# Kernel optimization log

Measured on AMD Instinct MI355X. Metric: run time of the kernel, lower is better.

Reference implementation:

```python
import jax, jax.numpy as jnp
import numpy as np

T_ENC = 80
MAX_LEN = 80
B = 64
D_IN = 4096
EU = 1024
DU = 1024
VOCAB = 20000
ATT = 80


def _lstm_scan(xs, h0, c0, W_ih, W_hh, b_ih, b_hh):
    """Single-layer LSTM over leading time dim. xs: [T,B,I]. Returns (ys[T,B,H], hT, cT)."""
    def step(carry, x):
        h, c = carry
        g = x @ W_ih.T + b_ih + h @ W_hh.T + b_hh
        i, f, gg, o = jnp.split(g, 4, axis=-1)
        c = jax.nn.sigmoid(f) * c + jax.nn.sigmoid(i) * jnp.tanh(gg)
        h = jax.nn.sigmoid(o) * jnp.tanh(c)
        return (h, c), h
    (hT, cT), ys = jax.lax.scan(step, (h0, c0), xs)
    return ys, hT, cT


def setup_inputs() -> dict:
    key = jax.random.key(0)
    ks = jax.random.split(key, 20)
    s = 0.05
    inp = {
        "input_data": jax.random.normal(ks[0], (T_ENC, B, D_IN), jnp.float32),
        "correct_answer": jax.random.normal(ks[1], (MAX_LEN, B, VOCAB), jnp.float32),
        # encoder LSTM params (torch gate order i,f,g,o)
        "enc_W_ih": jax.random.normal(ks[2], (4 * EU, D_IN), jnp.float32) * s,
        "enc_W_hh": jax.random.normal(ks[3], (4 * EU, EU), jnp.float32) * s,
        "enc_b_ih": jax.random.normal(ks[4], (4 * EU,), jnp.float32) * s,
        "enc_b_hh": jax.random.normal(ks[5], (4 * EU,), jnp.float32) * s,
        # decoder LSTM: input = decoder_unit + encoder_unit
        "dec_W_ih": jax.random.normal(ks[6], (4 * DU, DU + EU), jnp.float32) * s,
        "dec_W_hh": jax.random.normal(ks[7], (4 * DU, DU), jnp.float32) * s,
        "dec_b_ih": jax.random.normal(ks[8], (4 * DU,), jnp.float32) * s,
        "dec_b_hh": jax.random.normal(ks[9], (4 * DU,), jnp.float32) * s,
        # embeddings
        "in_emb_W": jax.random.normal(ks[10], (DU, VOCAB), jnp.float32) * s,
        "in_emb_b": jax.random.normal(ks[11], (DU,), jnp.float32) * s,
        "out_emb_W": jax.random.normal(ks[12], (VOCAB, DU), jnp.float32) * s,
        "out_emb_b": jax.random.normal(ks[13], (VOCAB,), jnp.float32) * s,
        # attention: linear_l1du_max ((d_l+1)*d_u -> 80), linear_2du_du (2*d_u -> d_u)
        "att_W1": jax.random.normal(ks[14], (ATT, 2 * DU), jnp.float32) * s,
        "att_b1": jax.random.normal(ks[15], (ATT,), jnp.float32) * s,
        "att_W2": jax.random.normal(ks[16], (DU, 2 * DU), jnp.float32) * s,
        "att_b2": jax.random.normal(ks[17], (DU,), jnp.float32) * s,
        "prelu_w": jnp.full((1,), 0.25, jnp.float32),  # PReLU(num_parameters=1) init
        "max_len": 80,
        "real_ans_length": jax.random.randint(ks[18], (B,), 0, 80),
    }
    return inp


def reference(input_data, correct_answer,
              enc_W_ih, enc_W_hh, enc_b_ih, enc_b_hh,
              dec_W_ih, dec_W_hh, dec_b_ih, dec_b_hh,
              in_emb_W, in_emb_b, out_emb_W, out_emb_b,
              att_W1, att_b1, att_W2, att_b2, prelu_w,
              max_len, real_ans_length):
    z_eh = jnp.zeros((B, EU), jnp.float32)
    z_dh = jnp.zeros((B, DU), jnp.float32)

    # encoding stage
    enc_seq, enc_h, enc_c = _lstm_scan(input_data, z_eh, z_eh, enc_W_ih, enc_W_hh, enc_b_ih, enc_b_hh)
    pad_tag = jnp.zeros((input_data.shape[0], B, DU), jnp.float32)
    dec_in0 = jnp.concatenate([enc_seq, pad_tag], axis=2)
    dec_out_seq, dec_h, dec_c = _lstm_scan(dec_in0, z_dh, z_dh, dec_W_ih, dec_W_hh, dec_b_ih, dec_b_hh)

    # encoder over zero padding inputs (continues encoder state)
    pad_in = jnp.zeros((max_len, B, D_IN), jnp.float32)
    enc_pad_seq, _, _ = _lstm_scan(pad_in, enc_h, enc_c, enc_W_ih, enc_W_hh, enc_b_ih, enc_b_hh)

    # teacher-forced samples (schedule_sample_rate == 1 -> always ground truth)
    bos = jnp.zeros((B, VOCAB), jnp.float32).at[:, -2].set(1.0)
    sample0 = bos @ in_emb_W.T + in_emb_b                              # [B, DU]
    samples_rest = correct_answer[1:max_len] @ in_emb_W.T + in_emb_b  # [max_len-1, B, DU]
    samples = jnp.concatenate([sample0[None], samples_rest], axis=0)   # [max_len, B, DU]

    E = enc_seq  # [80, B, EU]; attention weights have exactly 80 slots

    def dec_step(carry, inp):
        h, c = carry
        sample, enc_pad = inp
        # Attention: i = h (single layer), a = concat(i, word)
        a = jnp.concatenate([h, sample], axis=-1)          # [B, 2*DU]
        w = jax.nn.softmax(a @ att_W1.T + att_b1, axis=1)  # [B, 80]
        f = jnp.einsum('bs,sbh->bh', w, E)                 # [B, EU]
        cc = jnp.concatenate([sample, f], axis=-1)         # [B, 2*DU]
        z = cc @ att_W2.T + att_b2
        o = jnp.where(z >= 0, z, prelu_w[0] * z)           # PReLU (scalar param)
        context = o + enc_pad                              # [B, EU]
        x = jnp.concatenate([sample, context], axis=-1)    # [B, DU+EU]
        g = x @ dec_W_ih.T + dec_b_ih + h @ dec_W_hh.T + dec_b_hh
        gi, gf, gg, go = jnp.split(g, 4, axis=-1)
        c = jax.nn.sigmoid(gf) * c + jax.nn.sigmoid(gi) * jnp.tanh(gg)
        h = jax.nn.sigmoid(go) * jnp.tanh(c)
        word = h @ out_emb_W.T + out_emb_b                 # [B, VOCAB]
        return (h, c), word

    (_, _), words = jax.lax.scan(dec_step, (dec_h, dec_c), (samples, enc_pad_seq))
    return words  # [max_len, B, VOCAB]
```

## Files before the change

### kernel.cpp

```cpp
#include <hip/hip_runtime.h>
#include <cstddef>
#include <cstdint>

typedef __attribute__((ext_vector_type(8))) short short8v;
typedef __attribute__((ext_vector_type(4))) float f32x4;

__device__ __forceinline__ float sigmf(float x) { return 1.0f / (1.0f + __expf(-x)); }

__device__ __forceinline__ unsigned short bf16_rn(float x) {
    union { float f; unsigned u; } v; v.f = x;
    unsigned r = v.u + 0x7FFF + ((v.u >> 16) & 1);
    return (unsigned short)(r >> 16);
}
__device__ __forceinline__ float bf16_to_f(unsigned short h) {
    union { unsigned u; float f; } v; v.u = ((unsigned)h) << 16; return v.f;
}
__device__ __forceinline__ unsigned long long pack4(unsigned short a, unsigned short b,
                                                    unsigned short c, unsigned short d) {
    return (unsigned long long)a | ((unsigned long long)b << 16)
         | ((unsigned long long)c << 32) | ((unsigned long long)d << 48);
}

#define MFMA_(d, va, vb) d = __builtin_amdgcn_mfma_f32_16x16x32_bf16(va, vb, d, 0, 0, 0)

#define AT_LD(p)        __hip_atomic_load((p), __ATOMIC_RELAXED, __HIP_MEMORY_SCOPE_AGENT)
#define AT_ST(p, v)     __hip_atomic_store((p), (v), __ATOMIC_RELAXED, __HIP_MEMORY_SCOPE_AGENT)
#define AT_ST_REL(p, v) __hip_atomic_store((p), (v), __ATOMIC_RELEASE, __HIP_MEMORY_SCOPE_AGENT)
#define AT_ADD(p, v)    __hip_atomic_fetch_add((p), (v), __ATOMIC_RELAXED, __HIP_MEMORY_SCOPE_AGENT)

__device__ __forceinline__ void write_frag3_nt(unsigned short* __restrict__ dst, int NRGW,
                                               int r, int k, float x)
{
    unsigned short hi = bf16_rn(x); float r1 = x - bf16_to_f(hi);
    unsigned short md = bf16_rn(r1);
    unsigned short lo = bf16_rn(r1 - bf16_to_f(md));
    int base = (((r >> 4) * 32 + (k >> 5)) * 64 + ((k >> 3) & 3) * 16 + (r & 15)) * 8 + (k & 7);
    int ps = NRGW * 16384;
    __builtin_nontemporal_store(hi, &dst[base]);
    __builtin_nontemporal_store(md, &dst[ps + base]);
    __builtin_nontemporal_store(lo, &dst[2 * ps + base]);
}

__launch_bounds__(256)
__global__ void rearr_frag(const float* __restrict__ src, int ld, int c0,
                           unsigned short* __restrict__ dst, int R, int K)
{
    int idx = blockIdx.x * 256 + threadIdx.x;
    int kpr = K >> 3;
    if (idx >= R * kpr) return;
    int r = idx / kpr, k = (idx % kpr) * 8;
    int NRGW = R >> 4;
    const float* s = src + (size_t)r * ld + c0 + k;
    float4 v0 = *(const float4*)s, v1 = *(const float4*)(s + 4);
    float xs[8] = {v0.x, v0.y, v0.z, v0.w, v1.x, v1.y, v1.z, v1.w};
    unsigned short hi[8], md[8], lo[8];
#pragma unroll
    for (int e = 0; e < 8; ++e) {
        hi[e] = bf16_rn(xs[e]); float r1 = xs[e] - bf16_to_f(hi[e]);
        md[e] = bf16_rn(r1);
        lo[e] = bf16_rn(r1 - bf16_to_f(md[e]));
    }
    int base = (((r >> 4) * 32 + (k >> 5)) * 64 + ((k >> 3) & 3) * 16 + (r & 15)) * 8;
    size_t ps = (size_t)NRGW * 16384;
    *(unsigned long long*)&dst[base]          = pack4(hi[0], hi[1], hi[2], hi[3]);
    *(unsigned long long*)&dst[base + 4]      = pack4(hi[4], hi[5], hi[6], hi[7]);
    *(unsigned long long*)&dst[ps + base]     = pack4(md[0], md[1], md[2], md[3]);
    *(unsigned long long*)&dst[ps + base + 4] = pack4(md[4], md[5], md[6], md[7]);
    *(unsigned long long*)&dst[2*ps + base]     = pack4(lo[0], lo[1], lo[2], lo[3]);
    *(unsigned long long*)&dst[2*ps + base + 4] = pack4(lo[4], lo[5], lo[6], lo[7]);
}

__device__ __forceinline__ void tree_barrier(unsigned* bar, int gidx, int ng, int bpg)
{
    __syncthreads();
    if (threadIdx.x == 0) {
        unsigned* gcnt = bar + gidx * 32;
        unsigned* ggen = bar + gidx * 32 + 1;
        unsigned* rcnt = bar + ng * 32;
        unsigned* rgen = bar + ng * 32 + 1;
        __threadfence();
        unsigned mygen = AT_LD(ggen);
        unsigned prev = AT_ADD(gcnt, 1u);
        if (prev == (unsigned)(bpg - 1)) {
            AT_ST(gcnt, 0u);
            unsigned rg = AT_LD(rgen);
            unsigned rprev = AT_ADD(rcnt, 1u);
            if (rprev == (unsigned)(ng - 1)) {
                AT_ST(rcnt, 0u);
                AT_ST_REL(rgen, rg + 1u);
            } else {
                while (AT_LD(rgen) == rg) __builtin_amdgcn_s_sleep(1);
            }
            AT_ST_REL(ggen, mygen + 1u);
        } else {
            while (AT_LD(ggen) == mygen) __builtin_amdgcn_s_sleep(1);
        }
        __threadfence();
    }
    __syncthreads();
}

template <int NS>
__launch_bounds__(256, 2)
__global__ void gemm_mfma_split(const float* __restrict__ A, int lda,
                                const float* __restrict__ W, int ldw,
                                float* __restrict__ C, int ldc,
                                const float* __restrict__ bias,
                                int M, int N, int K)
{
    __shared__ unsigned short Abf[NS][128][40];
    __shared__ unsigned short Bbf[NS][128][40];
    const int tid = threadIdx.x;
    const int m0 = blockIdx.y * 128, n0 = blockIdx.x * 128;
    const int wave = tid >> 6, lane = tid & 63;
    const int wr = wave >> 1, wc = wave & 1;
    const int lr = lane & 15, lk = (lane >> 4) * 8;

    f32x4 acc[4][4];
#pragma unroll
    for (int i = 0; i < 4; ++i)
#pragma unroll
        for (int j = 0; j < 4; ++j) acc[i][j] = (f32x4){0.f, 0.f, 0.f, 0.f};

    const int arow = tid >> 1;
    const int akh  = (tid & 1) * 16;
    int gr = m0 + arow; if (gr > M - 1) gr = M - 1;
    int gn = n0 + arow; if (gn > N - 1) gn = N - 1;
    const float* aptr = A + (size_t)gr * lda + akh;
    const float* wptr = W + (size_t)gn * ldw + akh;

    for (int k0 = 0; k0 < K; k0 += 32) {
#pragma unroll
        for (int q = 0; q < 4; ++q) {
            float4 v = *(const float4*)(aptr + k0 + q * 4);
            float xs[4] = {v.x, v.y, v.z, v.w};
            unsigned short h[4], hm[4], hl[4];
#pragma unroll
            for (int e = 0; e < 4; ++e) {
                h[e] = bf16_rn(xs[e]);
                if (NS == 3) {
                    float r1 = xs[e] - bf16_to_f(h[e]);
                    hm[e] = bf16_rn(r1);
                    hl[e] = bf16_rn(r1 - bf16_to_f(hm[e]));
                }
            }
            *(unsigned long long*)&Abf[0][arow][akh + q * 4] = pack4(h[0], h[1], h[2], h[3]);
            if (NS == 3) {
                *(unsigned long long*)&Abf[1][arow][akh + q * 4] = pack4(hm[0], hm[1], hm[2], hm[3]);
                *(unsigned long long*)&Abf[2][arow][akh + q * 4] = pack4(hl[0], hl[1], hl[2], hl[3]);
            }
        }
#pragma unroll
        for (int q = 0; q < 4; ++q) {
            float4 v = *(const float4*)(wptr + k0 + q * 4);
            float xs[4] = {v.x, v.y, v.z, v.w};
            unsigned short h[4], hm[4], hl[4];
#pragma unroll
            for (int e = 0; e < 4; ++e) {
                h[e] = bf16_rn(xs[e]);
                if (NS == 3) {
                    float r1 = xs[e] - bf16_to_f(h[e]);
                    hm[e] = bf16_rn(r1);
                    hl[e] = bf16_rn(r1 - bf16_to_f(hm[e]));
                }
            }
            *(unsigned long long*)&Bbf[0][arow][akh + q * 4] = pack4(h[0], h[1], h[2], h[3]);
            if (NS == 3) {
                *(unsigned long long*)&Bbf[1][arow][akh + q * 4] = pack4(hm[0], hm[1], hm[2], hm[3]);
                *(unsigned long long*)&Bbf[2][arow][akh + q * 4] = pack4(hl[0], hl[1], hl[2], hl[3]);
            }
        }
        __syncthreads();

        short8v a[NS][4], b[4];
#pragma unroll
        for (int p = 0; p < NS; ++p)
#pragma unroll
            for (int i = 0; i < 4; ++i)
                a[p][i] = *(const short8v*)&Abf[p][wr * 64 + i * 16 + lr][lk];
#pragma unroll
        for (int q = 0; q < NS; ++q) {
#pragma unroll
            for (int j = 0; j < 4; ++j)
                b[j] = *(const short8v*)&Bbf[q][wc * 64 + j * 16 + lr][lk];
            const int pmax = (NS == 1) ? 1 : (3 - q);
#pragma unroll
            for (int p = 0; p < 3; ++p) {
                if (p >= pmax) break;
#pragma unroll
                for (int i = 0; i < 4; ++i)
#pragma unroll
                    for (int j = 0; j < 4; ++j)
                        acc[i][j] = __builtin_amdgcn_mfma_f32_16x16x32_bf16(
                            a[p][i], b[j], acc[i][j], 0, 0, 0);
            }
        }
        __syncthreads();
    }

    const int crow = (lane >> 4) * 4;
#pragma unroll
    for (int i = 0; i < 4; ++i) {
        int mbase = m0 + wr * 64 + i * 16 + crow;
#pragma unroll
        for (int j = 0; j < 4; ++j) {
            int n = n0 + wc * 64 + j * 16 + lr;
            if (n < N) {
                float bv = bias[n];
#pragma unroll
                for (int r = 0; r < 4; ++r) {
                    int m = mbase + r;
                    if (m < M) C[(size_t)m * ldc + n] = acc[i][j][r] + bv;
                }
            }
        }
    }
}

__launch_bounds__(256)
__global__ void zero_f(float* __restrict__ p, int n)
{
    int i = blockIdx.x * 256 + threadIdx.x;
    if (i < n) p[i] = 0.f;
}

__launch_bounds__(256)
__global__ void vec_add2(const float* __restrict__ a, const float* __restrict__ b,
                         float* __restrict__ o, int n)
{
    int i = blockIdx.x * 256 + threadIdx.x;
    if (i < n) o[i] = a[i] + b[i];
}

__launch_bounds__(256)
__global__ void sample0_fill(const float* __restrict__ emW, const float* __restrict__ emb,
                             float* __restrict__ samples)
{
    int idx = blockIdx.x * 256 + threadIdx.x;
    int d = idx & 1023;
    samples[idx] = emW[(size_t)d * 20000 + 19998] + emb[d];
}

__device__ __forceinline__ void stage_A(unsigned short* __restrict__ LDSA,
                                        const unsigned short* __restrict__ src,
                                        int rg, int tid)
{
#pragma unroll
    for (int p = 0; p < 3; ++p) {
        const unsigned short* sp = src + (size_t)(p * 4 + rg) * 16384;
        unsigned short* dp = LDSA + p * 16384;
#pragma unroll
        for (int it = 0; it < 4; ++it) {
            int idx = tid + it * 512;
            *(short8v*)&dp[idx * 8] = *(const short8v*)&sp[idx * 8];
        }
    }
}

__device__ __forceinline__ f32x4 mfma16(const unsigned short* __restrict__ LDSA,
                                        const short8v* __restrict__ wreg,
                                        int kh, int lane)
{
    f32x4 acc0 = (f32x4){0.f,0.f,0.f,0.f}, acc1 = acc0;
#pragma unroll
    for (int i = 0; i < 16; ++i) {
        int kf = kh * 16 + i;
        short8v a0 = *(const short8v*)&LDSA[(kf * 64 + lane) * 8];
        short8v a1 = *(const short8v*)&LDSA[16384 + (kf * 64 + lane) * 8];
        short8v a2 = *(const short8v*)&LDSA[32768 + (kf * 64 + lane) * 8];
        short8v b0 = wreg[i * 3 + 0], b1 = wreg[i * 3 + 1], b2 = wreg[i * 3 + 2];
        f32x4& A = (i & 1) ? acc1 : acc0;
        MFMA_(A, a0, b0); MFMA_(A, a0, b1); MFMA_(A, a1, b0);
        MFMA_(A, a1, b1); MFMA_(A, a0, b2); MFMA_(A, a2, b0);
    }
    return acc0 + acc1;
}

__launch_bounds__(512, 1)
__attribute__((amdgpu_waves_per_eu(1, 2)))
__global__ void coop_enc80(const unsigned short* __restrict__ WencF,
                           const float* __restrict__ Xbig,
                           unsigned short* __restrict__ hfrag,
                           float* __restrict__ enc_seq,
                           float* __restrict__ cglobE,
                           unsigned* __restrict__ bar)
{
    __shared__ unsigned short LDSA[3 * 16384];
    __shared__ float gbuf[8][16][16];
    const int bid = blockIdx.x, tid = threadIdx.x;
    const int w = tid >> 6, lane = tid & 63;
    const int g = w & 3, kh = w >> 2;
    const int rg = bid & 3, cg = bid >> 2;
    const int wbase = g * 64 + cg;
    const int r_l = (tid & 255) >> 4, c_l = tid & 15;
    const int row = rg * 16 + r_l, col = cg * 16 + c_l;
    float cstate = 0.f;

    short8v wreg[48];
#pragma unroll
    for (int i = 0; i < 16; ++i) {
        int kf = kh * 16 + i;
#pragma unroll
        for (int p = 0; p < 3; ++p)
            wreg[i * 3 + p] = *(const short8v*)&WencF[((size_t)(p * 256 + wbase) * 32 + kf) * 512 + lane * 8];
    }

    float pf[4];
    if (tid < 256) {
#pragma unroll
        for (int g2 = 0; g2 < 4; ++g2)
            pf[g2] = Xbig[(size_t)row * 4096 + g2 * 1024 + col];
    }

    for (int s = 0; s < 80; ++s) {
        const unsigned short* hf = hfrag + (s & 1) * 196608;
        stage_A(LDSA, hf, rg, tid);
        __syncthreads();
        f32x4 acc = mfma16(LDSA, wreg, kh, lane);
#pragma unroll
        for (int r = 0; r < 4; ++r)
            gbuf[w][(lane >> 4) * 4 + r][lane & 15] = acc[r];
        __syncthreads();

        if (tid < 256) {
            float gv[4];
#pragma unroll
            for (int g2 = 0; g2 < 4; ++g2)
                gv[g2] = gbuf[g2][r_l][c_l] + gbuf[4 + g2][r_l][c_l] + pf[g2];
            float cn = sigmf(gv[1]) * cstate + sigmf(gv[0]) * tanhf(gv[2]);
            float hn = sigmf(gv[3]) * tanhf(cn);
            cstate = cn;
            __builtin_nontemporal_store(hn, &enc_seq[(size_t)s * 65536 + row * 1024 + col]);
            write_frag3_nt(hfrag + ((s + 1) & 1) * 196608, 4, row, col, hn);
            if (s == 79) __builtin_nontemporal_store(cstate, &cglobE[row * 1024 + col]);
            else {
#pragma unroll
                for (int g2 = 0; g2 < 4; ++g2)
                    pf[g2] = Xbig[((size_t)(s + 1) * 64 + row) * 4096 + g2 * 1024 + col];
            }
        }
        tree_barrier(bar, bid >> 5, 8, 32);
    }
}

__launch_bounds__(512, 1)
__attribute__((amdgpu_waves_per_eu(1, 2)))
__global__ void coop_padwarm(const unsigned short* __restrict__ WencF,
                             const unsigned short* __restrict__ WdecF,
                             const float* __restrict__ benc,
                             const float* __restrict__ Xwarm,
                             const float* __restrict__ cglobE,
                             unsigned short* __restrict__ hfragE,
                             unsigned short* __restrict__ hfragD,
                             float* __restrict__ enc_pad,
                             float* __restrict__ cglobD,
                             float* __restrict__ h_fp32,
                             unsigned* __restrict__ barE,
                             unsigned* __restrict__ barW)
{
    __shared__ unsigned short LDSA[3 * 16384];
    __shared__ float gbuf[8][16][16];
    const int bid = blockIdx.x, tid = threadIdx.x;
    const int w = tid >> 6, lane = tid & 63;
    const int g = w & 3, kh = w >> 2;
    const bool isW = bid >= 128;
    const int lb = bid & 127;
    const int rg2 = lb & 1, cg = lb >> 1;
    const int wbase = g * 64 + cg;
    const int r_l = (tid & 255) >> 4, c_l = tid & 15;
    const int col = cg * 16 + c_l;
    const unsigned short* Wf = isW ? WdecF : WencF;
    unsigned short* hfrag = isW ? hfragD : hfragE;
    unsigned* bar = isW ? barW : barE;

    short8v wreg[48];
#pragma unroll
    for (int i = 0; i < 16; ++i) {
        int kf = kh * 16 + i;
#pragma unroll
        for (int p = 0; p < 3; ++p)
            wreg[i * 3 + p] = *(const short8v*)&Wf[((size_t)(p * 256 + wbase) * 32 + kf) * 512 + lane * 8];
    }

    float cst[2] = {0.f, 0.f};
    float pfx[2][4];
    if (tid < 256) {
#pragma unroll
        for (int l = 0; l < 2; ++l) {
            int row = rg2 * 32 + l * 16 + r_l;
            if (!isW) cst[l] = cglobE[row * 1024 + col];
#pragma unroll
            for (int g2 = 0; g2 < 4; ++g2)
                pfx[l][g2] = isW ? Xwarm[(size_t)row * 4096 + g2 * 1024 + col]
                                 : benc[g2 * 1024 + col];
        }
    }

    for (int s = 0; s < 80; ++s) {
        const unsigned short* hf = hfrag + (s & 1) * 196608;
        unsigned short* hout = hfrag + ((s + 1) & 1) * 196608;
#pragma unroll
        for (int l = 0; l < 2; ++l) {
            const int rgi = rg2 * 2 + l;
            stage_A(LDSA, hf, rgi, tid);
            __syncthreads();
            f32x4 acc = mfma16(LDSA, wreg, kh, lane);
#pragma unroll
            for (int r = 0; r < 4; ++r)
                gbuf[w][(lane >> 4) * 4 + r][lane & 15] = acc[r];
            __syncthreads();
            if (tid < 256) {
                const int row = rgi * 16 + r_l;
                float gv[4];
#pragma unroll
                for (int g2 = 0; g2 < 4; ++g2)
                    gv[g2] = gbuf[g2][r_l][c_l] + gbuf[4 + g2][r_l][c_l] + pfx[l][g2];
                float cn = sigmf(gv[1]) * cst[l] + sigmf(gv[0]) * tanhf(gv[2]);
                float hn = sigmf(gv[3]) * tanhf(cn);
                cst[l] = cn;
                if (!isW)
                    __builtin_nontemporal_store(hn, &enc_pad[(size_t)s * 65536 + row * 1024 + col]);
                write_frag3_nt(hout, 4, row, col, hn);
                if (isW) {
                    if (s == 79) {
                        __builtin_nontemporal_store(hn, &h_fp32[row * 1024 + col]);
                        __builtin_nontemporal_store(cn, &cglobD[row * 1024 + col]);
                    } else {
#pragma unroll
                        for (int g2 = 0; g2 < 4; ++g2)
                            pfx[l][g2] = Xwarm[((size_t)(s + 1) * 64 + row) * 4096 + g2 * 1024 + col];
                    }
                }
            }
            __syncthreads();
        }
        tree_barrier(bar, (lb >> 5), 4, 32);
    }
}

__launch_bounds__(512, 2)
__global__ void coop_dec80(const unsigned short* __restrict__ WihcF,
                           const unsigned short* __restrict__ WhhF,
                           const float* __restrict__ W1,
                           const float* __restrict__ EW2,
                           const float* __restrict__ S_g,
                           const float* __restrict__ ctxS,
                           const float* __restrict__ S_log,
                           const float* __restrict__ enc_pad,
                           const float* __restrict__ prelu_w,
                           const float* __restrict__ h_fp32,
                           const float* __restrict__ cglobD,
                           unsigned short* __restrict__ hfrag,
                           unsigned short* __restrict__ ctxfrag,
                           float* __restrict__ h_all,
                           float* __restrict__ gsum,
                           unsigned* __restrict__ bar)
{
    __shared__ float EW2T[80 * 256];
    __shared__ float gred[8][1024];
    __shared__ float hfull[1024];
    __shared__ float wsm[80];
    __shared__ float rbuf[128];
    const int bid = blockIdx.x, tid = threadIdx.x;
    const int w = tid >> 6, lane = tid & 63;
    const int gg = bid >> 6, cg = bid & 63;
    const int wbase = gg * 64 + cg;
    const int kq = w;
    const int b = bid >> 2, jc = bid & 3;
    const float pw = prelu_w[0];

    const unsigned short* Wsrc = (kq < 4) ? WihcF : WhhF;
    const int kfbase = (kq & 3) * 8;
    short8v wreg[24];
#pragma unroll
    for (int i = 0; i < 8; ++i) {
#pragma unroll
        for (int p = 0; p < 3; ++p)
            wreg[i * 3 + p] = *(const short8v*)&Wsrc[((size_t)(p * 256 + wbase) * 32 + kfbase + i) * 512 + lane * 8];
    }

    float c2[2];
    c2[0] = cglobD[b * 1024 + tid * 2];
    c2[1] = cglobD[b * 1024 + tid * 2 + 1];

    for (int i = tid; i < 80 * 256; i += 512) {
        int ss = i >> 8, j = i & 255;
        EW2T[i] = EW2[((size_t)ss * 64 + b) * 1024 + jc * 256 + j];
    }

    for (int i = tid; i < 1024; i += 512) hfull[i] = h_fp32[b * 1024 + i];
    __syncthreads();
    {
#pragma unroll
        for (int i = 0; i < 10; ++i) {
            int sx = w * 10 + i;
            float p = 0.f;
#pragma unroll
            for (int q = 0; q < 16; ++q)
                p = fmaf(hfull[lane + q * 64], W1[(size_t)sx * 2048 + lane + q * 64], p);
#pragma unroll
            for (int off = 32; off; off >>= 1) p += __shfl_down(p, off, 64);
            if (lane == 0) wsm[sx] = p + S_log[(size_t)b * 80 + sx];
        }
        __syncthreads();
        float v = (tid < 80) ? wsm[tid] : -3.4e38f;
        if (tid < 128) rbuf[tid] = v;
        __syncthreads();
        for (int off = 64; off >= 1; off >>= 1) {
            if (tid < off) rbuf[tid] = fmaxf(rbuf[tid], rbuf[tid + off]);
            __syncthreads();
        }
        float mx = rbuf[0];
        __syncthreads();
        float e = (tid < 80) ? __expf(wsm[tid] - mx) : 0.f;
        if (tid < 128) rbuf[tid] = e;
        __syncthreads();
        for (int off = 64; off >= 1; off >>= 1) {
            if (tid < off) rbuf[tid] += rbuf[tid + off];
            __syncthreads();
        }
        float inv = 1.f / rbuf[0];
        __syncthreads();
        if (tid < 80) wsm[tid] = e * inv;
        __syncthreads();
        if (tid < 256) {
            float f = 0.f;
#pragma unroll 8
            for (int ss = 0; ss < 80; ++ss)
                f = fmaf(wsm[ss], EW2T[ss * 256 + tid], f);
            int col = jc * 256 + tid;
            float val = f + ctxS[(size_t)b * 1024 + col];
            val = (val >= 0.f) ? val : pw * val;
            val += enc_pad[(size_t)b * 1024 + col];
            write_frag3_nt(ctxfrag, 4, b, col, val);
        }
    }
    tree_barrier(bar, bid >> 5, 8, 32);

    for (int t = 0; t < 80; ++t) {
        const int s = 80 + t;
        unsigned short* hout = hfrag + ((s + 1) & 1) * 196608;
        const unsigned short* hf = hfrag + (s & 1) * 196608;

        float pf2[2][4];
        {
            const float* xb = S_g + ((size_t)t * 64 + b) * 4096;
#pragma unroll
            for (int e = 0; e < 2; ++e) {
                int col = tid * 2 + e;
#pragma unroll
                for (int g2 = 0; g2 < 4; ++g2) pf2[e][g2] = xb[g2 * 1024 + col];
            }
        }

        {
            f32x4 acc[4];
#pragma unroll
            for (int rg = 0; rg < 4; ++rg) acc[rg] = (f32x4){0.f,0.f,0.f,0.f};
            const unsigned short* asrc = (kq < 4) ? ctxfrag : hf;
#pragma unroll
            for (int i = 0; i < 8; ++i) {
                int kfl = kfbase + i;
#pragma unroll
                for (int rg = 0; rg < 4; ++rg) {
                    const unsigned short* ab = asrc + ((size_t)rg * 32 + kfl) * 512 + lane * 8;
                    short8v a0 = *(const short8v*)&ab[0];
                    short8v a1 = *(const short8v*)&ab[65536];
                    short8v a2 = *(const short8v*)&ab[131072];
                    short8v b0 = wreg[i * 3 + 0], b1 = wreg[i * 3 + 1], b2 = wreg[i * 3 + 2];
                    MFMA_(acc[rg], a0, b0); MFMA_(acc[rg], a0, b1); MFMA_(acc[rg], a1, b0);
                    MFMA_(acc[rg], a1, b1); MFMA_(acc[rg], a0, b2); MFMA_(acc[rg], a2, b0);
                }
            }
#pragma unroll
            for (int rg = 0; rg < 4; ++rg)
#pragma unroll
                for (int r = 0; r < 4; ++r)
                    gred[w][rg * 256 + lane * 4 + r] = acc[rg][r];
            __syncthreads();
#pragma unroll
            for (int e2 = 0; e2 < 2; ++e2) {
                int slot = tid * 2 + e2;
                int rg = slot >> 8, l = (slot >> 2) & 63, r = slot & 3;
                float sum = 0.f;
#pragma unroll
                for (int w2 = 0; w2 < 8; ++w2) sum += gred[w2][slot];
                int row = rg * 16 + (l >> 4) * 4 + r;
                int col = cg * 16 + (l & 15);
                __builtin_nontemporal_store(sum, &gsum[((size_t)gg * 64 + row) * 1024 + col]);
            }
        }
        tree_barrier(bar, bid >> 5, 8, 32);

        {
            float hv[2];
#pragma unroll
            for (int e = 0; e < 2; ++e) {
                int col = tid * 2 + e;
                float gv[4];
#pragma unroll
                for (int g2 = 0; g2 < 4; ++g2)
                    gv[g2] = gsum[((size_t)g2 * 64 + b) * 1024 + col] + pf2[e][g2];
                float cn = sigmf(gv[1]) * c2[e] + sigmf(gv[0]) * tanhf(gv[2]);
                float hn = sigmf(gv[3]) * tanhf(cn);
                c2[e] = cn;
                hfull[col] = hn;
                hv[e] = hn;
            }
            __syncthreads();
            if (tid >= jc * 128 && tid < (jc + 1) * 128) {
#pragma unroll
                for (int e = 0; e < 2; ++e) {
                    int col = tid * 2 + e;
                    __builtin_nontemporal_store(hv[e], &h_all[((size_t)t * 64 + b) * 1024 + col]);
                    write_frag3_nt(hout, 4, b, col, hv[e]);
                }
            }
            if (t < 79) {
#pragma unroll
                for (int i = 0; i < 10; ++i) {
                    int sx = w * 10 + i;
                    float p = 0.f;
#pragma unroll
                    for (int q = 0; q < 16; ++q)
                        p = fmaf(hfull[lane + q * 64], W1[(size_t)sx * 2048 + lane + q * 64], p);
#pragma unroll
                    for (int off = 32; off; off >>= 1) p += __shfl_down(p, off, 64);
                    if (lane == 0) wsm[sx] = p + S_log[((size_t)(t + 1) * 64 + b) * 80 + sx];
                }
                __syncthreads();
                float v = (tid < 80) ? wsm[tid] : -3.4e38f;
                if (tid < 128) rbuf[tid] = v;
                __syncthreads();
                for (int off = 64; off >= 1; off >>= 1) {
                    if (tid < off) rbuf[tid] = fmaxf(rbuf[tid], rbuf[tid + off]);
                    __syncthreads();
                }
                float mx = rbuf[0];
                __syncthreads();
                float e = (tid < 80) ? __expf(wsm[tid] - mx) : 0.f;
                if (tid < 128) rbuf[tid] = e;
                __syncthreads();
                for (int off = 64; off >= 1; off >>= 1) {
                    if (tid < off) rbuf[tid] += rbuf[tid + off];
                    __syncthreads();
                }
                float inv = 1.f / rbuf[0];
                __syncthreads();
                if (tid < 80) wsm[tid] = e * inv;
                __syncthreads();
                if (tid < 256) {
                    float f = 0.f;
#pragma unroll 8
                    for (int ss = 0; ss < 80; ++ss)
                        f = fmaf(wsm[ss], EW2T[ss * 256 + tid], f);
                    int col = jc * 256 + tid;
                    float val = f + ctxS[((size_t)(t + 1) * 64 + b) * 1024 + col];
                    val = (val >= 0.f) ? val : pw * val;
                    val += enc_pad[((size_t)(t + 1) * 64 + b) * 1024 + col];
                    write_frag3_nt(ctxfrag, 4, b, col, val);
                }
            }
        }
        tree_barrier(bar, bid >> 5, 8, 32);
    }
}

extern "C" void kernel_launch(void* const* d_in, const int* in_sizes, int n_in,
                              void* d_out, int out_size, void* d_ws, size_t ws_size,
                              hipStream_t stream)
{
    (void)in_sizes; (void)n_in; (void)out_size; (void)ws_size;

    const float* input_data     = (const float*)d_in[0];
    const float* correct_answer = (const float*)d_in[1];
    const float* enc_W_ih = (const float*)d_in[2];
    const float* enc_W_hh = (const float*)d_in[3];
    const float* enc_b_ih = (const float*)d_in[4];
    const float* enc_b_hh = (const float*)d_in[5];
    const float* dec_W_ih = (const float*)d_in[6];
    const float* dec_W_hh = (const float*)d_in[7];
    const float* dec_b_ih = (const float*)d_in[8];
    const float* dec_b_hh = (const float*)d_in[9];
    const float* in_emb_W = (const float*)d_in[10];
    const float* in_emb_b = (const float*)d_in[11];
    const float* out_emb_W = (const float*)d_in[12];
    const float* out_emb_b = (const float*)d_in[13];
    const float* att_W1 = (const float*)d_in[14];
    const float* att_b1 = (const float*)d_in[15];
    const float* att_W2 = (const float*)d_in[16];
    const float* att_b2 = (const float*)d_in[17];
    const float* prelu_w = (const float*)d_in[18];

    float* out = (float*)d_out;
    char* ws = (char*)d_ws;

    float* Xbig    = out;
    float* S_g     = out + 20971520;
    float* ctxS    = out + 41943040;
    float* S_log   = out + 47185920;
    float* samples = out + 47595520;
    float* EW2     = out + 52838400;
    unsigned short* WencF = (unsigned short*)(out + 58081280);
    unsigned short* WhhDF = (unsigned short*)(out + 64372736);
    unsigned short* WihcF = (unsigned short*)(out + 70664192);

    size_t off = 0;
    auto alloc = [&](size_t nfloats) { float* p = (float*)(ws + off); off += nfloats * 4; return p; };
    float* enc_seq = alloc(80 * 64 * 1024);
    float* enc_pad = alloc(80 * 64 * 1024);
    float* h_all   = alloc(80 * 64 * 1024);
    float* benc    = alloc(4096);
    float* bdec    = alloc(4096);
    float* zb      = alloc(1024);
    float* hfragE_f = alloc(196608);
    float* hfragD_f = alloc(196608);
    float* ctxfrag_f= alloc(98304);
    float* gsum     = alloc(262144);
    float* cglobE   = alloc(65536);
    float* cglobD   = alloc(65536);
    float* h_fp32   = alloc(65536);
    float* bar_f    = alloc(2048);
    unsigned short* hfragE  = (unsigned short*)hfragE_f;
    unsigned short* hfragD  = (unsigned short*)hfragD_f;
    unsigned short* ctxfrag = (unsigned short*)ctxfrag_f;
    unsigned* barE1 = (unsigned*)bar_f;
    unsigned* barPE = ((unsigned*)bar_f) + 512;
    unsigned* barPW = ((unsigned*)bar_f) + 1024;
    unsigned* barD  = ((unsigned*)bar_f) + 1536;

    auto big3 = [&](const float* A, int lda, const float* W, int ldw,
                    float* C, int ldc, const float* bias, int M, int N, int K) {
        dim3 g((N + 127) / 128, (M + 127) / 128);
        hipLaunchKernelGGL((gemm_mfma_split<3>), g, dim3(256), 0, stream,
                           A, lda, W, ldw, C, ldc, bias, M, N, K);
    };

    hipLaunchKernelGGL(vec_add2, dim3(16), dim3(256), 0, stream, enc_b_ih, enc_b_hh, benc, 4096);
    hipLaunchKernelGGL(vec_add2, dim3(16), dim3(256), 0, stream, dec_b_ih, dec_b_hh, bdec, 4096);
    hipLaunchKernelGGL(zero_f, dim3(4), dim3(256), 0, stream, zb, 1024);
    hipLaunchKernelGGL(zero_f, dim3(768), dim3(256), 0, stream, hfragE_f, 196608);
    hipLaunchKernelGGL(zero_f, dim3(768), dim3(256), 0, stream, hfragD_f, 196608);
    hipLaunchKernelGGL(zero_f, dim3(8), dim3(256), 0, stream, bar_f, 2048);

    hipLaunchKernelGGL(rearr_frag, dim3(2048), dim3(256), 0, stream, enc_W_hh, 1024, 0, WencF, 4096, 1024);
    hipLaunchKernelGGL(rearr_frag, dim3(2048), dim3(256), 0, stream, dec_W_hh, 1024, 0, WhhDF, 4096, 1024);
    hipLaunchKernelGGL(rearr_frag, dim3(2048), dim3(256), 0, stream, dec_W_ih, 2048, 1024, WihcF, 4096, 1024);

    big3(input_data, 4096, enc_W_ih, 4096, Xbig, 4096, benc, 5120, 4096, 4096);
    hipLaunchKernelGGL(sample0_fill, dim3(256), dim3(256), 0, stream, in_emb_W, in_emb_b, samples);
    big3(correct_answer + (size_t)64 * 20000, 20000, in_emb_W, 20000,
         samples + 65536, 1024, in_emb_b, 5056, 1024, 20000);
    big3(samples, 1024, dec_W_ih, 2048, S_g, 4096, bdec, 5120, 4096, 1024);
    big3(samples, 1024, att_W2, 2048, ctxS, 1024, att_b2, 5120, 1024, 1024);
    big3(samples, 1024, att_W1 + 1024, 2048, S_log, 80, att_b1, 5120, 80, 1024);

    hipLaunchKernelGGL(coop_enc80, dim3(256), dim3(512), 0, stream,
                       WencF, Xbig, hfragE, enc_seq, cglobE, barE1);

    big3(enc_seq, 1024, dec_W_ih, 2048, Xbig, 4096, bdec, 5120, 4096, 1024);
    big3(enc_seq, 1024, att_W2 + 1024, 2048, EW2, 1024, zb, 5120, 1024, 1024);

    hipLaunchKernelGGL(coop_padwarm, dim3(256), dim3(512), 0, stream,
                       WencF, WhhDF, benc, Xbig, cglobE,
                       hfragE, hfragD, enc_pad, cglobD, h_fp32, barPE, barPW);

    hipLaunchKernelGGL(coop_dec80, dim3(256), dim3(512), 0, stream,
                       WihcF, WhhDF, att_W1, EW2, S_g, ctxS, S_log,
                       enc_pad, prelu_w, h_fp32, cglobD,
                       hfragD, ctxfrag, h_all, gsum, barD);

    {
        dim3 g((20000 + 127) / 128, (5120 + 127) / 128);
        hipLaunchKernelGGL((gemm_mfma_split<1>), g, dim3(256), 0, stream,
                           h_all, 1024, out_emb_W, 1024, out, 20000, out_emb_b, 5120, 20000, 1024);
    }
}
```

Baseline: 13.83 ms.

## Retile decoder gate GEMM so each block handles two column tiles and half the rows

Each decoder block now holds weights for two 16-column tiles in registers (48 fragments instead of 24) and processes only half the batch rows (2 row groups instead of 4). Every activation fragment loaded is therefore reused across two weight tiles, halving activation loads per MFMA. Launch bounds are relaxed to one block per SIMD group with waves_per_eu(1,2) to fit the larger register footprint, at the risk of lower occupancy and less latency hiding.

```diff
diff --git a/kernel.cpp b/kernel.cpp
--- a/kernel.cpp
+++ b/kernel.cpp
@@ -438,7 +438,8 @@
     }
 }
 
-__launch_bounds__(512, 2)
+__launch_bounds__(512, 1)
+__attribute__((amdgpu_waves_per_eu(1, 2)))
 __global__ void coop_dec80(const unsigned short* __restrict__ WihcF,
                            const unsigned short* __restrict__ WhhF,
                            const float* __restrict__ W1,
@@ -463,20 +464,24 @@
     __shared__ float rbuf[128];
     const int bid = blockIdx.x, tid = threadIdx.x;
     const int w = tid >> 6, lane = tid & 63;
-    const int gg = bid >> 6, cg = bid & 63;
-    const int wbase = gg * 64 + cg;
+    const int rp = bid & 1, u = bid >> 1;
     const int kq = w;
     const int b = bid >> 2, jc = bid & 3;
     const float pw = prelu_w[0];
 
     const unsigned short* Wsrc = (kq < 4) ? WihcF : WhhF;
     const int kfbase = (kq & 3) * 8;
-    short8v wreg[24];
-#pragma unroll
-    for (int i = 0; i < 8; ++i) {
-#pragma unroll
-        for (int p = 0; p < 3; ++p)
-            wreg[i * 3 + p] = *(const short8v*)&Wsrc[((size_t)(p * 256 + wbase) * 32 + kfbase + i) * 512 + lane * 8];
+    short8v wreg[48];
+#pragma unroll
+    for (int ct = 0; ct < 2; ++ct) {
+        const int wbase2 = u * 2 + ct;
+#pragma unroll
+        for (int i = 0; i < 8; ++i) {
+#pragma unroll
+            for (int p = 0; p < 3; ++p)
+                wreg[(ct * 8 + i) * 3 + p] =
+                    *(const short8v*)&Wsrc[((size_t)(p * 256 + wbase2) * 32 + kfbase + i) * 512 + lane * 8];
+        }
     }
 
     float c2[2];
@@ -554,40 +559,53 @@
         }
 
         {
-            f32x4 acc[4];
-#pragma unroll
-            for (int rg = 0; rg < 4; ++rg) acc[rg] = (f32x4){0.f,0.f,0.f,0.f};
+            f32x4 acc[2][2];
+#pragma unroll
+            for (int rgl = 0; rgl < 2; ++rgl)
+#pragma unroll
+                for (int ct = 0; ct < 2; ++ct) acc[rgl][ct] = (f32x4){0.f,0.f,0.f,0.f};
             const unsigned short* asrc = (kq < 4) ? ctxfrag : hf;
 #pragma unroll
             for (int i = 0; i < 8; ++i) {
                 int kfl = kfbase + i;
 #pragma unroll
-                for (int rg = 0; rg < 4; ++rg) {
+                for (int rgl = 0; rgl < 2; ++rgl) {
+                    const int rg = rp * 2 + rgl;
                     const unsigned short* ab = asrc + ((size_t)rg * 32 + kfl) * 512 + lane * 8;
                     short8v a0 = *(const short8v*)&ab[0];
                     short8v a1 = *(const short8v*)&ab[65536];
                     short8v a2 = *(const short8v*)&ab[131072];
-                    short8v b0 = wreg[i * 3 + 0], b1 = wreg[i * 3 + 1], b2 = wreg[i * 3 + 2];
-                    MFMA_(acc[rg], a0, b0); MFMA_(acc[rg], a0, b1); MFMA_(acc[rg], a1, b0);
-                    MFMA_(acc[rg], a1, b1); MFMA_(acc[rg], a0, b2); MFMA_(acc[rg], a2, b0);
-                }
-            }
-#pragma unroll
-            for (int rg = 0; rg < 4; ++rg)
-#pragma unroll
-                for (int r = 0; r < 4; ++r)
-                    gred[w][rg * 256 + lane * 4 + r] = acc[rg][r];
+#pragma unroll
+                    for (int ct = 0; ct < 2; ++ct) {
+                        short8v b0 = wreg[(ct * 8 + i) * 3 + 0];
+                        short8v b1 = wreg[(ct * 8 + i) * 3 + 1];
+                        short8v b2 = wreg[(ct * 8 + i) * 3 + 2];
+                        MFMA_(acc[rgl][ct], a0, b0); MFMA_(acc[rgl][ct], a0, b1);
+                        MFMA_(acc[rgl][ct], a1, b0); MFMA_(acc[rgl][ct], a1, b1);
+                        MFMA_(acc[rgl][ct], a0, b2); MFMA_(acc[rgl][ct], a2, b0);
+                    }
+                }
+            }
+#pragma unroll
+            for (int rgl = 0; rgl < 2; ++rgl)
+#pragma unroll
+                for (int ct = 0; ct < 2; ++ct)
+#pragma unroll
+                    for (int r = 0; r < 4; ++r)
+                        gred[w][(rgl * 2 + ct) * 256 + lane * 4 + r] = acc[rgl][ct][r];
             __syncthreads();
 #pragma unroll
             for (int e2 = 0; e2 < 2; ++e2) {
                 int slot = tid * 2 + e2;
-                int rg = slot >> 8, l = (slot >> 2) & 63, r = slot & 3;
+                int t4 = slot >> 8, l = (slot >> 2) & 63, r = slot & 3;
                 float sum = 0.f;
 #pragma unroll
                 for (int w2 = 0; w2 < 8; ++w2) sum += gred[w2][slot];
-                int row = rg * 16 + (l >> 4) * 4 + r;
-                int col = cg * 16 + (l & 15);
-                __builtin_nontemporal_store(sum, &gsum[((size_t)gg * 64 + row) * 1024 + col]);
+                int rgl = t4 >> 1, ct = t4 & 1;
+                int row = rp * 32 + rgl * 16 + (l >> 4) * 4 + r;
+                int fr = (u * 2 + ct) * 16 + (l & 15);
+                __builtin_nontemporal_store(sum,
+                    &gsum[((size_t)(fr >> 10) * 64 + row) * 1024 + (fr & 1023)]);
             }
         }
         tree_barrier(bar, bid >> 5, 8, 32);
```

New measurement: 16.41 ms. +18.6%, slower.
